# Performance work log

Measured on AMD Instinct MI355X. Metric: run time of the kernel, lower is better.

The kernel has to match this reference:

```python
import jax, jax.numpy as jnp
import numpy as np

ORDER = 2
C_IN = 32
C_OUT = 32
SUPPORT_LEN = 2


def setup_inputs() -> dict:
    key = jax.random.key(0)
    k1, k2, k3, k4 = jax.random.split(key, 4)
    B, C, V, L = 32, C_IN, 2048, 12
    x = jax.random.normal(k1, (B, C, V, L), dtype=jnp.float32)
    supports = jax.random.uniform(k2, (SUPPORT_LEN, V, V), dtype=jnp.float32) / V
    c_cat = (ORDER * SUPPORT_LEN + 1) * C_IN
    W = jax.random.normal(k3, (C_OUT, c_cat), dtype=jnp.float32) * (1.0 / np.sqrt(c_cat))
    b = jax.random.normal(k4, (C_OUT,), dtype=jnp.float32) * 0.01
    return {"x": x, "supports": supports, "W": W, "b": b}


def reference(x, supports, W, b):
    # x: [B, C, V, L]; supports: [S, V, V]; W: [c_out, (order*S+1)*C]; b: [c_out]
    out = [x]
    for s in range(supports.shape[0]):  # fixed small S
        A = supports[s]
        x1 = jnp.einsum('bcvl,vw->bcwl', x, A)
        out.append(x1)
        for _ in range(ORDER - 1):
            x1 = jnp.einsum('bcvl,vw->bcwl', x1, A)
            out.append(x1)
    h = jnp.concatenate(out, axis=1)  # [B, (order*S+1)*C, V, L]
    # 1x1 conv == channel-mixing matmul; dropout is identity in eval mode
    y = jnp.einsum('bcvl,oc->bovl', h, W) + b[None, :, None, None]
    return y
```

## Files before the change

kernel.cpp:

```cpp
#include <hip/hip_runtime.h>

#define BB 32
#define CC 32
#define VV 2048
#define LL 12
#define NCOL 12288
#define MMEGA 8192

typedef __attribute__((ext_vector_type(8))) short bf16x8;
typedef __attribute__((ext_vector_type(4))) float f32x4;

__device__ __forceinline__ unsigned short f2b(float f) {
    union { float f; unsigned u; } v; v.f = f;
    unsigned u = v.u;
    unsigned r = (u + 0x7fffu + ((u >> 16) & 1u)) >> 16;
    return (unsigned short)r;
}
__device__ __forceinline__ float b2f(unsigned short h) {
    union { unsigned u; float f; } v; v.u = ((unsigned)h) << 16;
    return v.f;
}

__device__ __forceinline__ void stg(const unsigned short* g, unsigned short* l) {
    __builtin_amdgcn_global_load_lds((const __attribute__((address_space(1))) void*)g,
                                     (__attribute__((address_space(3))) void*)l, 16, 0, 0);
}

__global__ void k_convert_bf16(const float* __restrict__ src,
                               unsigned short* __restrict__ dst) {
    size_t i = (size_t)(blockIdx.x * blockDim.x + threadIdx.x) * 4;
    float4 v = *(const float4*)(src + i);
    ushort4 o; o.x = f2b(v.x); o.y = f2b(v.y); o.z = f2b(v.z); o.w = f2b(v.w);
    *(ushort4*)(dst + i) = o;
}

__global__ void k_transpose_A(const float* __restrict__ A,
                              unsigned short* __restrict__ Gt) {
    __shared__ float t[32][33];
    const int s = blockIdx.z;
    const float* As = A + (size_t)s * VV * VV;
    const int w0 = blockIdx.x * 32, v0 = blockIdx.y * 32;
    const int tid = threadIdx.x;
    const int cc = tid & 31;
#pragma unroll
    for (int i = 0; i < 4; i++) {
        int rr = (tid >> 5) + i * 8;
        t[rr][cc] = As[(size_t)(v0 + rr) * VV + w0 + cc];
    }
    __syncthreads();
    unsigned short* G = Gt + (size_t)(2 * s) * VV * VV;
#pragma unroll
    for (int i = 0; i < 4; i++) {
        int rr = (tid >> 5) + i * 8;
        G[(size_t)(w0 + rr) * VV + v0 + cc] = f2b(t[cc][rr]);
    }
}

__global__ void k_transpose_x(const float* __restrict__ x,
                              unsigned short* __restrict__ Xb) {
    __shared__ float t[128 * 13];
    const int bc = blockIdx.y;
    const int v0 = blockIdx.x * 128;
    const float* xs = x + (size_t)bc * VV * LL + (size_t)v0 * LL;
    const int tid = threadIdx.x;
#pragma unroll
    for (int i = 0; i < 6; i++) {
        int e = tid + i * 256;
        int col = e / 12, row = e - col * 12;
        t[col * 13 + row] = xs[e];
    }
    __syncthreads();
    unsigned short* X = Xb + (size_t)bc * LL * VV + v0;
#pragma unroll
    for (int i = 0; i < 6; i++) {
        int e = tid + i * 256;
        int row = e >> 7, col = e & 127;
        X[(size_t)row * VV + col] = f2b(t[col * 13 + row]);
    }
}

__global__ __launch_bounds__(512, 2) void k_gemm8(
    const unsigned short* __restrict__ Ag, const unsigned short* __restrict__ Bg,
    unsigned short* __restrict__ Cg, int K, int ldc,
    size_t aStr, size_t bStr, size_t cStr)
{
    __shared__ unsigned short SH[65536];
    const int tid  = threadIdx.x;
    const int lane = tid & 63;
    const int wid  = tid >> 6;
    const int wr   = wid >> 2;
    const int wc   = wid & 3;
    const int fr   = lane & 15;
    const int g    = lane >> 4;
    const int NT   = K >> 6;

    const int m0 = blockIdx.y * 256;
    const int n0 = blockIdx.x * 256;
    const unsigned short* gA = Ag + blockIdx.z * aStr + (size_t)m0 * K;
    const unsigned short* gB = Bg + blockIdx.z * bStr + (size_t)n0 * K;
    unsigned short* gC = Cg + blockIdx.z * cStr;

    const int lrow  = lane >> 3;
    const int lslot = (lane & 7) ^ lrow;
    const size_t laneGOff = (size_t)lrow * K + lslot * 8;

    const int qa  = wid * 16;
    const int rA0 = (qa & 63) + ((qa & 64) << 1);
    const int rA1 = ((qa + 8) & 63) + (((qa + 8) & 64) << 1);
    const int rB0 = (qa & 31) + ((qa & ~31) << 1);
    const int rB1 = ((qa + 8) & 31) + (((qa + 8) & ~31) << 1);

    const int frlow = fr & 7;
    const int sw0 = ((0 + g) ^ frlow) << 4;
    const int sw1 = ((4 + g) ^ frlow) << 4;
    const int aOffB = (wr * 128 + fr) * 128;
    const int bOffB = (wc * 64  + fr) * 128;

    f32x4 acc[8][4];
#pragma unroll
    for (int i = 0; i < 8; ++i)
#pragma unroll
        for (int j = 0; j < 4; ++j) { f32x4 z = {0.f, 0.f, 0.f, 0.f}; acc[i][j] = z; }

#define STG_A(Lb, rb, kt) stg(gA + (size_t)(rb) * K + ((size_t)(kt) << 6) + laneGOff, (Lb) + (rb) * 64)
#define STG_B(Lb, rb, kt) stg(gB + (size_t)(rb) * K + ((size_t)(kt) << 6) + laneGOff, (Lb) + (rb) * 64)
#define ST_Aa(Lb, kt) do { if ((kt) < NT) { STG_A(Lb, rA0, kt);      STG_A(Lb, rA1, kt);      } } while (0)
#define ST_Ab(Lb, kt) do { if ((kt) < NT) { STG_A(Lb, rA0 + 64, kt); STG_A(Lb, rA1 + 64, kt); } } while (0)
#define ST_Ba(Lb, kt) do { if ((kt) < NT) { STG_B(Lb, rB0, kt);      STG_B(Lb, rB1, kt);      } } while (0)
#define ST_Bb(Lb, kt) do { if ((kt) < NT) { STG_B(Lb, rB0 + 32, kt); STG_B(Lb, rB1 + 32, kt); } } while (0)
#define VM6() asm volatile("s_waitcnt vmcnt(6)" ::: "memory")
#define VM0() asm volatile("s_waitcnt vmcnt(0)" ::: "memory")
#define LGKM0() asm volatile("s_waitcnt lgkmcnt(0)" ::: "memory")
#define SBAR() __builtin_amdgcn_s_barrier()

    unsigned short* A0L = SH;
    unsigned short* B0L = SH + 16384;
    unsigned short* A1L = SH + 32768;
    unsigned short* B1L = SH + 49152;

    ST_Aa(A0L, 0); ST_Ab(A0L, 0); ST_Ba(B0L, 0); ST_Bb(B0L, 0);
    ST_Aa(A1L, 1); ST_Ab(A1L, 1); ST_Ba(B1L, 1);
    if (NT > 1) { VM6(); } else { VM0(); }
    SBAR();

    bf16x8 aM0[4][2], aM1[4][2], bN[2][2];

    for (int t = 0; t < NT; ++t) {
        const char* Ab = (const char*)(SH + ((t & 1) << 15));
        const char* Bb = Ab + 32768;
        unsigned short* An = SH + (((t + 1) & 1) << 15);
        unsigned short* Bn = An + 16384;
        unsigned short* Ac = SH + ((t & 1) << 15);
        unsigned short* Bc = Ac + 16384;

#pragma unroll
        for (int i = 0; i < 4; ++i) {
            aM0[i][0] = *(const bf16x8*)(Ab + aOffB + i * 2048 + sw0);
            aM0[i][1] = *(const bf16x8*)(Ab + aOffB + i * 2048 + sw1);
        }
#pragma unroll
        for (int j = 0; j < 2; ++j) {
            bN[j][0] = *(const bf16x8*)(Bb + bOffB + j * 2048 + sw0);
            bN[j][1] = *(const bf16x8*)(Bb + bOffB + j * 2048 + sw1);
        }
        ST_Bb(Bn, t + 1);
        SBAR(); LGKM0();
        __builtin_amdgcn_s_setprio(1);
#pragma unroll
        for (int i = 0; i < 4; ++i)
#pragma unroll
            for (int j = 0; j < 2; ++j) {
                acc[i][j] = __builtin_amdgcn_mfma_f32_16x16x32_bf16(aM0[i][0], bN[j][0], acc[i][j], 0, 0, 0);
                acc[i][j] = __builtin_amdgcn_mfma_f32_16x16x32_bf16(aM0[i][1], bN[j][1], acc[i][j], 0, 0, 0);
            }
        __builtin_amdgcn_s_setprio(0);
        SBAR();

#pragma unroll
        for (int i = 0; i < 4; ++i) {
            aM1[i][0] = *(const bf16x8*)(Ab + aOffB + 8192 + i * 2048 + sw0);
            aM1[i][1] = *(const bf16x8*)(Ab + aOffB + 8192 + i * 2048 + sw1);
        }
        ST_Aa(Ac, t + 2);
        SBAR(); LGKM0();
        __builtin_amdgcn_s_setprio(1);
#pragma unroll
        for (int i = 0; i < 4; ++i)
#pragma unroll
            for (int j = 0; j < 2; ++j) {
                acc[4 + i][j] = __builtin_amdgcn_mfma_f32_16x16x32_bf16(aM1[i][0], bN[j][0], acc[4 + i][j], 0, 0, 0);
                acc[4 + i][j] = __builtin_amdgcn_mfma_f32_16x16x32_bf16(aM1[i][1], bN[j][1], acc[4 + i][j], 0, 0, 0);
            }
        __builtin_amdgcn_s_setprio(0);
        SBAR();

#pragma unroll
        for (int j = 0; j < 2; ++j) {
            bN[j][0] = *(const bf16x8*)(Bb + bOffB + 4096 + j * 2048 + sw0);
            bN[j][1] = *(const bf16x8*)(Bb + bOffB + 4096 + j * 2048 + sw1);
        }
        ST_Ab(Ac, t + 2);
        SBAR(); LGKM0();
        __builtin_amdgcn_s_setprio(1);
#pragma unroll
        for (int i = 0; i < 4; ++i)
#pragma unroll
            for (int j = 0; j < 2; ++j) {
                acc[i][2 + j] = __builtin_amdgcn_mfma_f32_16x16x32_bf16(aM0[i][0], bN[j][0], acc[i][2 + j], 0, 0, 0);
                acc[i][2 + j] = __builtin_amdgcn_mfma_f32_16x16x32_bf16(aM0[i][1], bN[j][1], acc[i][2 + j], 0, 0, 0);
            }
        __builtin_amdgcn_s_setprio(0);
        SBAR();

        ST_Ba(Bc, t + 2);
        if (t + 2 < NT) { VM6(); } else { VM0(); }
        SBAR();
        __builtin_amdgcn_s_setprio(1);
#pragma unroll
        for (int i = 0; i < 4; ++i)
#pragma unroll
            for (int j = 0; j < 2; ++j) {
                acc[4 + i][2 + j] = __builtin_amdgcn_mfma_f32_16x16x32_bf16(aM1[i][0], bN[j][0], acc[4 + i][2 + j], 0, 0, 0);
                acc[4 + i][2 + j] = __builtin_amdgcn_mfma_f32_16x16x32_bf16(aM1[i][1], bN[j][1], acc[4 + i][2 + j], 0, 0, 0);
            }
        __builtin_amdgcn_s_setprio(0);
        SBAR();
    }

    const int er = g * 4;
#pragma unroll
    for (int i = 0; i < 8; ++i)
#pragma unroll
        for (int j = 0; j < 4; ++j) {
            int row = m0 + wr * 128 + i * 16 + er;
            int col = n0 + wc * 64 + j * 16 + fr;
#pragma unroll
            for (int r = 0; r < 4; ++r)
                gC[(size_t)(row + r) * ldc + col] = f2b(acc[i][j][r]);
        }
#undef STG_A
#undef STG_B
#undef ST_Aa
#undef ST_Ab
#undef ST_Ba
#undef ST_Bb
#undef VM6
#undef VM0
#undef LGKM0
#undef SBAR
}

__global__ __launch_bounds__(192) void k_epilogue(const float* __restrict__ x,
                                                  const unsigned short* __restrict__ U,
                                                  const float* __restrict__ W,
                                                  const float* __restrict__ bias,
                                                  float* __restrict__ y) {
    __shared__ float xs[32][192];
    __shared__ unsigned short us[64][392];
    const int b = blockIdx.y;
    const int w0 = blockIdx.x * 16;
    const int tid = threadIdx.x;

    const float* xp = x + ((size_t)(b * 32) * VV + w0) * LL;
#pragma unroll 4
    for (int c = 0; c < 32; c++)
        xs[c][tid] = xp[(size_t)c * (VV * LL) + tid];

    for (int kk = 0; kk < 64; kk++) {
        int krow = (kk >> 4) * VV + w0 + (kk & 15);
        const unsigned short* up = U + (size_t)krow * NCOL + b * 384;
        *(ushort2*)&us[kk][tid * 2] = *(const ushort2*)&up[tid * 2];
    }
    __syncthreads();

    const int w = tid / 12, l = tid - w * 12;
    float acc[32];
#pragma unroll
    for (int o = 0; o < 32; o++) acc[o] = bias[o];

    for (int c = 0; c < 32; c++) {
        float h = xs[c][tid];
#pragma unroll
        for (int o = 0; o < 32; o++) acc[o] += W[o * 160 + c] * h;
    }
    for (int c = 0; c < 32; c++) {
#pragma unroll
        for (int k = 0; k < 4; k++) {
            float h = b2f(us[k * 16 + w][c * 12 + l]);
#pragma unroll
            for (int o = 0; o < 32; o++) acc[o] += W[o * 160 + (k + 1) * 32 + c] * h;
        }
    }

    float* yp = y + ((size_t)(b * 32) * VV + w0) * LL;
#pragma unroll
    for (int o = 0; o < 32; o++)
        yp[(size_t)o * (VV * LL) + tid] = acc[o];
}

extern "C" void kernel_launch(void* const* d_in, const int* in_sizes, int n_in,
                              void* d_out, int out_size, void* d_ws, size_t ws_size,
                              hipStream_t stream) {
    const float* x        = (const float*)d_in[0];
    const float* supports = (const float*)d_in[1];
    const float* W        = (const float*)d_in[2];
    const float* bias     = (const float*)d_in[3];
    float* y = (float*)d_out;

    char* ws = (char*)d_ws;
    unsigned short* Xb  = (unsigned short*)(ws);
    unsigned short* Gt  = (unsigned short*)(ws + 50331648);
    unsigned short* Abf = (unsigned short*)(ws + 83886080);
    unsigned short* U   = (unsigned short*)(ws + 100663296);

    const size_t VB = (size_t)VV * VV;

    k_convert_bf16<<<dim3((2 * VB) / 1024), 256, 0, stream>>>(supports, Abf);

    k_transpose_A<<<dim3(64, 64, 2), 256, 0, stream>>>(supports, Gt);

    k_gemm8<<<dim3(8, 8, 2), 512, 0, stream>>>(Gt, Abf, Gt + VB, VV, VV,
                                               2 * VB, VB, 2 * VB);

    k_transpose_x<<<dim3(16, 1024), 256, 0, stream>>>(x, Xb);

    k_gemm8<<<dim3(NCOL / 256, MMEGA / 256, 1), 512, 0, stream>>>(Gt, Xb, U, VV, NCOL,
                                                                  0, 0, 0);

    k_epilogue<<<dim3(VV / 16, BB), 192, 0, stream>>>(x, U, W, bias, y);
}
```

Before: 914.9 us.

## Fuse A prep kernels, prefetch LDS fragments in GEMM, vectorize stores/loads

Merges the bf16 conversion and transpose of the supports into one kernel so the fp32 supports are read once. Restructures the GEMM main loop to double-register fragments, prefetching the next tile's A/B fragments during the last MFMA phase and using partial lgkmcnt waits plus sched barriers so LDS reads overlap with MFMA. Also vectorizes the x transpose stores to ushort4 and the epilogue U loads to 16-byte loads. The extra fragment registers raise register pressure under the 2-blocks-per-CU launch bound, and the hand-counted lgkmcnt values must match the issued LDS reads.

```diff
diff --git a/kernel.cpp b/kernel.cpp
--- a/kernel.cpp
+++ b/kernel.cpp
@@ -26,26 +26,22 @@
                                      (__attribute__((address_space(3))) void*)l, 16, 0, 0);
 }
 
-__global__ void k_convert_bf16(const float* __restrict__ src,
-                               unsigned short* __restrict__ dst) {
-    size_t i = (size_t)(blockIdx.x * blockDim.x + threadIdx.x) * 4;
-    float4 v = *(const float4*)(src + i);
-    ushort4 o; o.x = f2b(v.x); o.y = f2b(v.y); o.z = f2b(v.z); o.w = f2b(v.w);
-    *(ushort4*)(dst + i) = o;
-}
-
-__global__ void k_transpose_A(const float* __restrict__ A,
-                              unsigned short* __restrict__ Gt) {
+__global__ void k_prepA(const float* __restrict__ A,
+                        unsigned short* __restrict__ Abf,
+                        unsigned short* __restrict__ Gt) {
     __shared__ float t[32][33];
     const int s = blockIdx.z;
     const float* As = A + (size_t)s * VV * VV;
     const int w0 = blockIdx.x * 32, v0 = blockIdx.y * 32;
     const int tid = threadIdx.x;
     const int cc = tid & 31;
+    unsigned short* Ao = Abf + (size_t)s * VV * VV;
 #pragma unroll
     for (int i = 0; i < 4; i++) {
         int rr = (tid >> 5) + i * 8;
-        t[rr][cc] = As[(size_t)(v0 + rr) * VV + w0 + cc];
+        float val = As[(size_t)(v0 + rr) * VV + w0 + cc];
+        t[rr][cc] = val;
+        Ao[(size_t)(v0 + rr) * VV + w0 + cc] = f2b(val);
     }
     __syncthreads();
     unsigned short* G = Gt + (size_t)(2 * s) * VV * VV;
@@ -72,10 +68,18 @@
     __syncthreads();
     unsigned short* X = Xb + (size_t)bc * LL * VV + v0;
 #pragma unroll
-    for (int i = 0; i < 6; i++) {
-        int e = tid + i * 256;
-        int row = e >> 7, col = e & 127;
-        X[(size_t)row * VV + col] = f2b(t[col * 13 + row]);
+    for (int i = 0; i < 2; i++) {
+        int flat = tid + i * 256;
+        if (flat < 384) {
+            int row = flat >> 5;
+            int col = (flat & 31) * 4;
+            ushort4 o;
+            o.x = f2b(t[(col + 0) * 13 + row]);
+            o.y = f2b(t[(col + 1) * 13 + row]);
+            o.z = f2b(t[(col + 2) * 13 + row]);
+            o.w = f2b(t[(col + 3) * 13 + row]);
+            *(ushort4*)&X[(size_t)row * VV + col] = o;
+        }
     }
 }
 
@@ -130,7 +134,8 @@
 #define ST_Bb(Lb, kt) do { if ((kt) < NT) { STG_B(Lb, rB0 + 32, kt); STG_B(Lb, rB1 + 32, kt); } } while (0)
 #define VM6() asm volatile("s_waitcnt vmcnt(6)" ::: "memory")
 #define VM0() asm volatile("s_waitcnt vmcnt(0)" ::: "memory")
-#define LGKM0() asm volatile("s_waitcnt lgkmcnt(0)" ::: "memory")
+#define LGKM(n) asm volatile("s_waitcnt lgkmcnt(" #n ")" ::: "memory")
+#define SCHB() __builtin_amdgcn_sched_barrier(0)
 #define SBAR() __builtin_amdgcn_s_barrier()
 
     unsigned short* A0L = SH;
@@ -143,71 +148,78 @@
     if (NT > 1) { VM6(); } else { VM0(); }
     SBAR();
 
-    bf16x8 aM0[4][2], aM1[4][2], bN[2][2];
+    bf16x8 aA[4][2], aB[4][2], b0[2][2], b1[2][2];
+    {
+        const char* Ab = (const char*)SH;
+        const char* Bb = Ab + 32768;
+#pragma unroll
+        for (int i = 0; i < 4; ++i) {
+            aA[i][0] = *(const bf16x8*)(Ab + aOffB + i * 2048 + sw0);
+            aA[i][1] = *(const bf16x8*)(Ab + aOffB + i * 2048 + sw1);
+        }
+#pragma unroll
+        for (int j = 0; j < 2; ++j) {
+            b0[j][0] = *(const bf16x8*)(Bb + bOffB + j * 2048 + sw0);
+            b0[j][1] = *(const bf16x8*)(Bb + bOffB + j * 2048 + sw1);
+        }
+    }
 
     for (int t = 0; t < NT; ++t) {
-        const char* Ab = (const char*)(SH + ((t & 1) << 15));
-        const char* Bb = Ab + 32768;
+        const char* Ab  = (const char*)(SH + ((t & 1) << 15));
+        const char* Bb  = Ab + 32768;
+        const char* AbN = (const char*)(SH + (((t + 1) & 1) << 15));
+        const char* BbN = AbN + 32768;
         unsigned short* An = SH + (((t + 1) & 1) << 15);
         unsigned short* Bn = An + 16384;
         unsigned short* Ac = SH + ((t & 1) << 15);
         unsigned short* Bc = Ac + 16384;
+        (void)An;
 
 #pragma unroll
         for (int i = 0; i < 4; ++i) {
-            aM0[i][0] = *(const bf16x8*)(Ab + aOffB + i * 2048 + sw0);
-            aM0[i][1] = *(const bf16x8*)(Ab + aOffB + i * 2048 + sw1);
-        }
-#pragma unroll
-        for (int j = 0; j < 2; ++j) {
-            bN[j][0] = *(const bf16x8*)(Bb + bOffB + j * 2048 + sw0);
-            bN[j][1] = *(const bf16x8*)(Bb + bOffB + j * 2048 + sw1);
+            aB[i][0] = *(const bf16x8*)(Ab + aOffB + 8192 + i * 2048 + sw0);
+            aB[i][1] = *(const bf16x8*)(Ab + aOffB + 8192 + i * 2048 + sw1);
         }
         ST_Bb(Bn, t + 1);
-        SBAR(); LGKM0();
+        SBAR(); LGKM(8); SCHB();
         __builtin_amdgcn_s_setprio(1);
 #pragma unroll
         for (int i = 0; i < 4; ++i)
 #pragma unroll
             for (int j = 0; j < 2; ++j) {
-                acc[i][j] = __builtin_amdgcn_mfma_f32_16x16x32_bf16(aM0[i][0], bN[j][0], acc[i][j], 0, 0, 0);
-                acc[i][j] = __builtin_amdgcn_mfma_f32_16x16x32_bf16(aM0[i][1], bN[j][1], acc[i][j], 0, 0, 0);
+                acc[i][j] = __builtin_amdgcn_mfma_f32_16x16x32_bf16(aA[i][0], b0[j][0], acc[i][j], 0, 0, 0);
+                acc[i][j] = __builtin_amdgcn_mfma_f32_16x16x32_bf16(aA[i][1], b0[j][1], acc[i][j], 0, 0, 0);
             }
         __builtin_amdgcn_s_setprio(0);
         SBAR();
 
 #pragma unroll
-        for (int i = 0; i < 4; ++i) {
-            aM1[i][0] = *(const bf16x8*)(Ab + aOffB + 8192 + i * 2048 + sw0);
-            aM1[i][1] = *(const bf16x8*)(Ab + aOffB + 8192 + i * 2048 + sw1);
+        for (int j = 0; j < 2; ++j) {
+            b1[j][0] = *(const bf16x8*)(Bb + bOffB + 4096 + j * 2048 + sw0);
+            b1[j][1] = *(const bf16x8*)(Bb + bOffB + 4096 + j * 2048 + sw1);
         }
         ST_Aa(Ac, t + 2);
-        SBAR(); LGKM0();
+        SBAR(); LGKM(4); SCHB();
         __builtin_amdgcn_s_setprio(1);
 #pragma unroll
         for (int i = 0; i < 4; ++i)
 #pragma unroll
             for (int j = 0; j < 2; ++j) {
-                acc[4 + i][j] = __builtin_amdgcn_mfma_f32_16x16x32_bf16(aM1[i][0], bN[j][0], acc[4 + i][j], 0, 0, 0);
-                acc[4 + i][j] = __builtin_amdgcn_mfma_f32_16x16x32_bf16(aM1[i][1], bN[j][1], acc[4 + i][j], 0, 0, 0);
+                acc[4 + i][j] = __builtin_amdgcn_mfma_f32_16x16x32_bf16(aB[i][0], b0[j][0], acc[4 + i][j], 0, 0, 0);
+                acc[4 + i][j] = __builtin_amdgcn_mfma_f32_16x16x32_bf16(aB[i][1], b0[j][1], acc[4 + i][j], 0, 0, 0);
             }
         __builtin_amdgcn_s_setprio(0);
         SBAR();
 
-#pragma unroll
-        for (int j = 0; j < 2; ++j) {
-            bN[j][0] = *(const bf16x8*)(Bb + bOffB + 4096 + j * 2048 + sw0);
-            bN[j][1] = *(const bf16x8*)(Bb + bOffB + 4096 + j * 2048 + sw1);
-        }
         ST_Ab(Ac, t + 2);
-        SBAR(); LGKM0();
+        SBAR(); LGKM(0); SCHB();
         __builtin_amdgcn_s_setprio(1);
 #pragma unroll
         for (int i = 0; i < 4; ++i)
 #pragma unroll
             for (int j = 0; j < 2; ++j) {
-                acc[i][2 + j] = __builtin_amdgcn_mfma_f32_16x16x32_bf16(aM0[i][0], bN[j][0], acc[i][2 + j], 0, 0, 0);
-                acc[i][2 + j] = __builtin_amdgcn_mfma_f32_16x16x32_bf16(aM0[i][1], bN[j][1], acc[i][2 + j], 0, 0, 0);
+                acc[i][2 + j] = __builtin_amdgcn_mfma_f32_16x16x32_bf16(aA[i][0], b1[j][0], acc[i][2 + j], 0, 0, 0);
+                acc[i][2 + j] = __builtin_amdgcn_mfma_f32_16x16x32_bf16(aA[i][1], b1[j][1], acc[i][2 + j], 0, 0, 0);
             }
         __builtin_amdgcn_s_setprio(0);
         SBAR();
@@ -215,13 +227,24 @@
         ST_Ba(Bc, t + 2);
         if (t + 2 < NT) { VM6(); } else { VM0(); }
         SBAR();
+#pragma unroll
+        for (int i = 0; i < 4; ++i) {
+            aA[i][0] = *(const bf16x8*)(AbN + aOffB + i * 2048 + sw0);
+            aA[i][1] = *(const bf16x8*)(AbN + aOffB + i * 2048 + sw1);
+        }
+#pragma unroll
+        for (int j = 0; j < 2; ++j) {
+            b0[j][0] = *(const bf16x8*)(BbN + bOffB + j * 2048 + sw0);
+            b0[j][1] = *(const bf16x8*)(BbN + bOffB + j * 2048 + sw1);
+        }
+        LGKM(12); SCHB();
         __builtin_amdgcn_s_setprio(1);
 #pragma unroll
         for (int i = 0; i < 4; ++i)
 #pragma unroll
             for (int j = 0; j < 2; ++j) {
-                acc[4 + i][2 + j] = __builtin_amdgcn_mfma_f32_16x16x32_bf16(aM1[i][0], bN[j][0], acc[4 + i][2 + j], 0, 0, 0);
-                acc[4 + i][2 + j] = __builtin_amdgcn_mfma_f32_16x16x32_bf16(aM1[i][1], bN[j][1], acc[4 + i][2 + j], 0, 0, 0);
+                acc[4 + i][2 + j] = __builtin_amdgcn_mfma_f32_16x16x32_bf16(aB[i][0], b1[j][0], acc[4 + i][2 + j], 0, 0, 0);
+                acc[4 + i][2 + j] = __builtin_amdgcn_mfma_f32_16x16x32_bf16(aB[i][1], b1[j][1], acc[4 + i][2 + j], 0, 0, 0);
             }
         __builtin_amdgcn_s_setprio(0);
         SBAR();
@@ -246,7 +269,8 @@
 #undef ST_Bb
 #undef VM6
 #undef VM0
-#undef LGKM0
+#undef LGKM
+#undef SCHB
 #undef SBAR
 }
 
@@ -266,10 +290,16 @@
     for (int c = 0; c < 32; c++)
         xs[c][tid] = xp[(size_t)c * (VV * LL) + tid];
 
-    for (int kk = 0; kk < 64; kk++) {
-        int krow = (kk >> 4) * VV + w0 + (kk & 15);
-        const unsigned short* up = U + (size_t)krow * NCOL + b * 384;
-        *(ushort2*)&us[kk][tid * 2] = *(const ushort2*)&up[tid * 2];
+    {
+        const int r0 = tid / 48;
+        const int c0 = tid - r0 * 48;
+#pragma unroll
+        for (int it = 0; it < 16; ++it) {
+            int r = it * 4 + r0;
+            int krow = (r >> 4) * VV + w0 + (r & 15);
+            const unsigned short* up = U + (size_t)krow * NCOL + b * 384 + c0 * 8;
+            *(bf16x8*)&us[r][c0 * 8] = *(const bf16x8*)up;
+        }
     }
     __syncthreads();
 
@@ -315,9 +345,7 @@
 
     const size_t VB = (size_t)VV * VV;
 
-    k_convert_bf16<<<dim3((2 * VB) / 1024), 256, 0, stream>>>(supports, Abf);
-
-    k_transpose_A<<<dim3(64, 64, 2), 256, 0, stream>>>(supports, Gt);
+    k_prepA<<<dim3(64, 64, 2), 256, 0, stream>>>(supports, Abf, Gt);
 
     k_gemm8<<<dim3(8, 8, 2), 512, 0, stream>>>(Gt, Abf, Gt + VB, VV, VV,
                                                2 * VB, VB, 2 * VB);
```

Measured after the change: 850.0 us. -7.1%, faster.
